# Performance work log

Measured on AMD Instinct MI355X. Metric: run time of the kernel, lower is better.

Reference implementation:

```python
import jax, jax.numpy as jnp
import numpy as np

B, C, H, W, K = 8, 256, 128, 128, 19  # batch, image channels, spatial, num keypoints


def _uniform_linear(key, out_dim, in_dim):
    # torch nn.Linear default init: U(-1/sqrt(fan_in), 1/sqrt(fan_in))
    bound = 1.0 / np.sqrt(in_dim)
    kw, kb = jax.random.split(key)
    w = jax.random.uniform(kw, (out_dim, in_dim), jnp.float32, -bound, bound)
    b = jax.random.uniform(kb, (out_dim,), jnp.float32, -bound, bound)
    return w, b


def setup_inputs() -> dict:
    key = jax.random.key(0)
    ks = jax.random.split(key, 8)
    image_features = jax.random.normal(ks[0], (B, C, H, W), jnp.float32)
    # keypoints: (x, y, vis). forward computes int((x / W).clamp(0, W-1)), so
    # coords are drawn in [0, W*W) / [0, H*H) to cover the full heatmap grid.
    kx = jax.random.uniform(ks[1], (B, K), jnp.float32, 0.0, float(W * W))
    ky = jax.random.uniform(ks[2], (B, K), jnp.float32, 0.0, float(H * H))
    vis = jax.random.uniform(ks[3], (B, K), jnp.float32)  # >0 => visible
    keypoint_features = jnp.stack([kx, ky, vis], axis=-1)  # [B,K,3]
    img_fc_w, img_fc_b = _uniform_linear(ks[4], C, C)
    kp_proj_w, kp_proj_b = _uniform_linear(ks[5], K, K)  # 1x1 conv == K->K linear over channels
    kp_fc_w, kp_fc_b = _uniform_linear(ks[6], C, K)
    attn_fc_w, attn_fc_b = _uniform_linear(ks[7], 1, C)
    return {
        "image_features": image_features,
        "keypoint_features": keypoint_features,
        "img_fc_w": img_fc_w, "img_fc_b": img_fc_b,
        "kp_proj_w": kp_proj_w, "kp_proj_b": kp_proj_b,
        "kp_fc_w": kp_fc_w, "kp_fc_b": kp_fc_b,
        "attn_fc_w": attn_fc_w, "attn_fc_b": attn_fc_b,
    }


def keypoints_to_heatmap(keypoints, Hh, Ww):
    # Vectorized version of the original nested Python double-loop scatter.
    bsz, nkp, _ = keypoints.shape
    vis = (keypoints[:, :, 2] > 0).astype(jnp.float32)            # [B,K]
    # clamp to [0, dim-1] then truncate to int (values are >=0 so floor==trunc)
    x = jnp.clip(keypoints[:, :, 0] / Ww, 0.0, Ww - 1).astype(jnp.int32)  # [B,K]
    y = jnp.clip(keypoints[:, :, 1] / Hh, 0.0, Hh - 1).astype(jnp.int32)  # [B,K]
    bi = jnp.arange(bsz)[:, None]
    ki = jnp.arange(nkp)[None, :]
    heatmap = jnp.zeros((bsz, nkp, Hh, Ww), jnp.float32)
    # one write per (b,k) -> indices unique across writes; add of 0 for invisible kp
    return heatmap.at[bi, ki, y, x].add(vis)


def reference(image_features, keypoint_features,
              img_fc_w, img_fc_b, kp_proj_w, kp_proj_b,
              kp_fc_w, kp_fc_b, attn_fc_w, attn_fc_b):
    bsz, nch, Hh, Ww = image_features.shape
    heatmap = keypoints_to_heatmap(keypoint_features, Hh, Ww)  # [B,K,H,W]
    # F.interpolate to the same (H,W) with bilinear/align_corners=False maps
    # output pixel i -> input coord i exactly => identity; no-op.
    # keypoint_proj: 1x1 conv over K channels == per-pixel K->K linear
    kp_feat = jnp.einsum('bkhw,ok->bohw', heatmap, kp_proj_w) + kp_proj_b[None, :, None, None]
    img = image_features.reshape(bsz, nch, Hh * Ww).transpose(0, 2, 1)   # [B,S,C]
    kp = kp_feat.reshape(bsz, K, Hh * Ww).transpose(0, 2, 1)             # [B,S,K]
    img_proj = jnp.einsum('bsc,oc->bso', img, img_fc_w) + img_fc_b       # [B,S,C]
    kp_proj = jnp.einsum('bsk,ok->bso', kp, kp_fc_w) + kp_fc_b           # [B,S,C]
    combined = jnp.tanh(img_proj + kp_proj)
    scores = jax.nn.sigmoid(jnp.einsum('bsc,oc->bso', combined, attn_fc_w) + attn_fc_b)  # [B,S,1]
    attended = img * scores                                              # [B,S,C]
    return attended.transpose(0, 2, 1).reshape(bsz, nch, Hh, Ww)
```

## Files before the change

### kernel.cpp

```cpp
#include <hip/hip_runtime.h>
#include <hip/hip_bf16.h>

#define CCH 256
#define HH 128
#define WW 128
#define SS (HH*WW)
#define NB 8
#define NK 19
#define STILE 64

typedef __attribute__((ext_vector_type(8))) short short8v;
typedef __attribute__((ext_vector_type(4))) float f32x4;

static __device__ __forceinline__ unsigned short f2bf(float x) {
    __hip_bfloat16 h = __float2bfloat16(x);
    return *reinterpret_cast<unsigned short*>(&h);
}
static __device__ __forceinline__ float bf2f(unsigned short u) {
    union { unsigned int i; float f; } z; z.i = ((unsigned int)u) << 16; return z.f;
}
static __device__ __forceinline__ float tanh_fast(float x) {
    float e = __expf(2.f * x);
    return 1.f - 2.f / (e + 1.f);
}

__global__ __launch_bounds__(256) void precompute_kernel(
    const float* __restrict__ kf,
    const float* __restrict__ img_fc_w,
    const float* __restrict__ img_fc_b,
    const float* __restrict__ kp_proj_w,
    const float* __restrict__ kp_proj_b,
    const float* __restrict__ kp_fc_w,
    const float* __restrict__ kp_fc_b,
    float* __restrict__ cb,
    float* __restrict__ delta,
    int* __restrict__ pix,
    unsigned short* __restrict__ Wfrag)
{
    int t = threadIdx.x;
    {
        float acc = img_fc_b[t] + kp_fc_b[t];
        for (int k2 = 0; k2 < NK; ++k2) acc += kp_fc_w[t * NK + k2] * kp_proj_b[k2];
        cb[t] = acc;
        for (int k = 0; k < NK; ++k) {
            float d = 0.f;
            for (int k2 = 0; k2 < NK; ++k2) d += kp_fc_w[t * NK + k2] * kp_proj_w[k2 * NK + k];
            delta[t * NK + k] = d;
        }
    }
    if (t < NB * NK) {
        float kx = kf[t * 3 + 0], ky = kf[t * 3 + 1], vis = kf[t * 3 + 2];
        int p = -1;
        if (vis > 0.f) {
            int xi = (int)fminf(fmaxf(kx * (1.f / (float)WW), 0.f), (float)(WW - 1));
            int yi = (int)fminf(fmaxf(ky * (1.f / (float)HH), 0.f), (float)(HH - 1));
            p = yi * WW + xi;
        }
        pix[t] = p;
    }
    for (int g = t; g < 8 * 16 * 64; g += 256) {
        int lane = g & 63;
        int ot = (g >> 6) & 15;
        int ks = g >> 10;
        int o = ot * 16 + (lane & 15);
        int c0 = ks * 32 + (lane >> 4) * 8;
#pragma unroll
        for (int j = 0; j < 8; ++j)
            Wfrag[g * 8 + j] = f2bf(img_fc_w[o * CCH + c0 + j]);
    }
}

__global__ __launch_bounds__(256) void main_kernel(
    const float* __restrict__ img,
    const unsigned short* __restrict__ Wfrag,
    const float* __restrict__ cb,
    const float* __restrict__ aw,
    const float* __restrict__ attn_b,
    float* __restrict__ out)
{
    __shared__ unsigned short Xl[64 * 256];
    __shared__ float tmp[64 * 68];
    __shared__ float partial[4][64];
    __shared__ float scl[64];

    const int t = threadIdx.x;
    const int l = t & 63;
    const int w = t >> 6;
    const int bid = blockIdx.x;
    const int b = bid >> 8;
    const int sb = (bid & 255) * STILE;
    const float* imgb = img + (size_t)b * CCH * SS;

    for (int cc = 0; cc < 4; ++cc) {
#pragma unroll
        for (int it = 0; it < 4; ++it) {
            int idx = t + it * 256;
            int c = idx >> 4;
            int sq = idx & 15;
            const float4 v = *reinterpret_cast<const float4*>(
                imgb + (size_t)(cc * 64 + c) * SS + sb + sq * 4);
            *reinterpret_cast<float4*>(&tmp[c * 68 + sq * 4]) = v;
        }
        __syncthreads();
        {
            int s = t & 63;
            int tr = t >> 6;
#pragma unroll
            for (int half = 0; half < 2; ++half) {
                int c0 = tr * 16 + half * 8;
                short8v pk;
#pragma unroll
                for (int j = 0; j < 8; ++j)
                    pk[j] = (short)f2bf(tmp[(c0 + j) * 68 + s]);
                int cglob = cc * 64 + c0;
                int cblk = cglob >> 3;
                int idx = s * 256 + ((cblk ^ (s & 7)) << 3);
                *reinterpret_cast<short8v*>(&Xl[idx]) = pk;
            }
        }
        __syncthreads();
    }

    f32x4 acc[4][4];
#pragma unroll
    for (int m = 0; m < 4; ++m)
#pragma unroll
        for (int n = 0; n < 4; ++n)
            acc[m][n] = (f32x4){0.f, 0.f, 0.f, 0.f};

    for (int ks = 0; ks < 8; ++ks) {
        short8v a[4], bf[4];
#pragma unroll
        for (int m = 0; m < 4; ++m) {
            int ot = w * 4 + m;
            a[m] = *reinterpret_cast<const short8v*>(
                &Wfrag[(((ks * 16 + ot) * 64) + l) * 8]);
        }
#pragma unroll
        for (int n = 0; n < 4; ++n) {
            int s = n * 16 + (l & 15);
            int cblk = ks * 4 + (l >> 4);
            int idx = s * 256 + ((cblk ^ (s & 7)) << 3);
            bf[n] = *reinterpret_cast<const short8v*>(&Xl[idx]);
        }
#pragma unroll
        for (int m = 0; m < 4; ++m)
#pragma unroll
            for (int n = 0; n < 4; ++n)
                acc[m][n] = __builtin_amdgcn_mfma_f32_16x16x32_bf16(a[m], bf[n], acc[m][n], 0, 0, 0);
    }

    float cbv[4][4], awv[4][4];
#pragma unroll
    for (int m = 0; m < 4; ++m)
#pragma unroll
        for (int r = 0; r < 4; ++r) {
            int o = w * 64 + m * 16 + ((l >> 4) << 2) + r;
            cbv[m][r] = cb[o];
            awv[m][r] = aw[o];
        }
    float p[4];
#pragma unroll
    for (int n = 0; n < 4; ++n) {
        float acc_p = 0.f;
#pragma unroll
        for (int m = 0; m < 4; ++m)
#pragma unroll
            for (int r = 0; r < 4; ++r)
                acc_p += awv[m][r] * tanh_fast(acc[m][n][r] + cbv[m][r]);
        acc_p += __shfl_xor(acc_p, 16);
        acc_p += __shfl_xor(acc_p, 32);
        p[n] = acc_p;
    }
    if (l < 16) {
#pragma unroll
        for (int n = 0; n < 4; ++n) partial[w][n * 16 + l] = p[n];
    }
    __syncthreads();
    if (t < 64) {
        float z = partial[0][t] + partial[1][t] + partial[2][t] + partial[3][t] + attn_b[0];
        scl[t] = 1.f / (1.f + __expf(-z));
    }
    __syncthreads();

    float sc = scl[l];
#pragma unroll
    for (int g = 0; g < 8; ++g) {
        int cg = w * 64 + g * 8;
        int cblk = cg >> 3;
        int idx = l * 256 + ((cblk ^ (l & 7)) << 3);
        short8v v = *reinterpret_cast<const short8v*>(&Xl[idx]);
#pragma unroll
        for (int j = 0; j < 8; ++j) {
            float xv = bf2f((unsigned short)v[j]);
            out[(size_t)(b * CCH + cg + j) * SS + sb + l] = xv * sc;
        }
    }
}

__global__ __launch_bounds__(256) void fixup_kernel(
    const float* __restrict__ img,
    const float* __restrict__ img_fc_w,
    const float* __restrict__ aw,
    const float* __restrict__ attn_b,
    const float* __restrict__ cb,
    const float* __restrict__ delta,
    const int* __restrict__ pix,
    float* __restrict__ out)
{
    int bk = blockIdx.x;
    int b = bk / NK;
    int p = pix[bk];
    if (p < 0) return;
    __shared__ float x[256];
    __shared__ float red[256];
    __shared__ float ssc;
    int t = threadIdx.x;
    const float* imgb = img + (size_t)b * CCH * SS;
    x[t] = imgb[(size_t)t * SS + p];
    __syncthreads();
    float dsum = 0.f;
    for (int k2 = 0; k2 < NK; ++k2)
        if (pix[b * NK + k2] == p) dsum += delta[t * NK + k2];
    float acc = cb[t] + dsum;
    for (int c = 0; c < CCH; ++c) acc += img_fc_w[t * CCH + c] * x[c];
    red[t] = aw[t] * tanh_fast(acc);
    __syncthreads();
    for (int off = 128; off > 0; off >>= 1) {
        if (t < off) red[t] += red[t + off];
        __syncthreads();
    }
    if (t == 0) ssc = 1.f / (1.f + __expf(-(red[0] + attn_b[0])));
    __syncthreads();
    out[(size_t)(b * CCH + t) * SS + p] = x[t] * ssc;
}

extern "C" void kernel_launch(void* const* d_in, const int* in_sizes, int n_in,
                              void* d_out, int out_size, void* d_ws, size_t ws_size,
                              hipStream_t stream) {
    (void)in_sizes; (void)n_in; (void)out_size; (void)ws_size;
    const float* img       = (const float*)d_in[0];
    const float* kf        = (const float*)d_in[1];
    const float* img_fc_w  = (const float*)d_in[2];
    const float* img_fc_b  = (const float*)d_in[3];
    const float* kp_proj_w = (const float*)d_in[4];
    const float* kp_proj_b = (const float*)d_in[5];
    const float* kp_fc_w   = (const float*)d_in[6];
    const float* kp_fc_b   = (const float*)d_in[7];
    const float* attn_fc_w = (const float*)d_in[8];
    const float* attn_fc_b = (const float*)d_in[9];
    float* out = (float*)d_out;

    char* ws = (char*)d_ws;
    float* cb            = (float*)(ws);
    float* delta         = (float*)(ws + 1024);
    int*   pix           = (int*)  (ws + 20480);
    unsigned short* Wfrag = (unsigned short*)(ws + 21504);

    precompute_kernel<<<1, 256, 0, stream>>>(kf, img_fc_w, img_fc_b, kp_proj_w,
                                             kp_proj_b, kp_fc_w, kp_fc_b,
                                             cb, delta, pix, Wfrag);
    main_kernel<<<NB * (SS / STILE), 256, 0, stream>>>(img, Wfrag, cb,
                                                       attn_fc_w, attn_fc_b, out);
    fixup_kernel<<<NB * NK, 256, 0, stream>>>(img, img_fc_w, attn_fc_w, attn_fc_b,
                                              cb, delta, pix, out);
}
```

Measured before the change: 94.30 us.

## Double block size, prefetch whole image tile into registers, write fp32 output directly

The main kernel now runs 512 threads (8 waves) per block, each wave covering 32 output channels instead of 64. All global loads of the 64x256 image tile are issued up front into registers, so the whole tile is in flight at once instead of being fetched per chunk. The kept fp32 values are then reused for the final scaling with coalesced float4 stores, rather than reading back the bf16 copy. This also removes the bf16 rounding from the output. The cost is higher register pressure (32 floats held across the GEMM) and a larger reduction over 8 partial sums.

Result: slower. 99.17 us (+5.2%).

```diff
diff --git a/kernel.cpp b/kernel.cpp
--- a/kernel.cpp
+++ b/kernel.cpp
@@ -15,9 +15,6 @@
 static __device__ __forceinline__ unsigned short f2bf(float x) {
     __hip_bfloat16 h = __float2bfloat16(x);
     return *reinterpret_cast<unsigned short*>(&h);
-}
-static __device__ __forceinline__ float bf2f(unsigned short u) {
-    union { unsigned int i; float f; } z; z.i = ((unsigned int)u) << 16; return z.f;
 }
 static __device__ __forceinline__ float tanh_fast(float x) {
     float e = __expf(2.f * x);
@@ -70,7 +67,7 @@
     }
 }
 
-__global__ __launch_bounds__(256) void main_kernel(
+__global__ __launch_bounds__(512, 4) void main_kernel(
     const float* __restrict__ img,
     const unsigned short* __restrict__ Wfrag,
     const float* __restrict__ cb,
@@ -80,7 +77,7 @@
 {
     __shared__ unsigned short Xl[64 * 256];
     __shared__ float tmp[64 * 68];
-    __shared__ float partial[4][64];
+    __shared__ float partial[8][64];
     __shared__ float scl[64];
 
     const int t = threadIdx.x;
@@ -91,48 +88,51 @@
     const int sb = (bid & 255) * STILE;
     const float* imgb = img + (size_t)b * CCH * SS;
 
+    float4 xv[4][2];
+#pragma unroll
+    for (int cc = 0; cc < 4; ++cc)
+#pragma unroll
+        for (int it = 0; it < 2; ++it) {
+            int idx = t + it * 512;
+            xv[cc][it] = *reinterpret_cast<const float4*>(
+                imgb + (size_t)(cc * 64 + (idx >> 4)) * SS + sb + (idx & 15) * 4);
+        }
+
+#pragma unroll
     for (int cc = 0; cc < 4; ++cc) {
 #pragma unroll
-        for (int it = 0; it < 4; ++it) {
-            int idx = t + it * 256;
-            int c = idx >> 4;
-            int sq = idx & 15;
-            const float4 v = *reinterpret_cast<const float4*>(
-                imgb + (size_t)(cc * 64 + c) * SS + sb + sq * 4);
-            *reinterpret_cast<float4*>(&tmp[c * 68 + sq * 4]) = v;
+        for (int it = 0; it < 2; ++it) {
+            int idx = t + it * 512;
+            *reinterpret_cast<float4*>(&tmp[(idx >> 4) * 68 + (idx & 15) * 4]) = xv[cc][it];
         }
         __syncthreads();
         {
-            int s = t & 63;
-            int tr = t >> 6;
-#pragma unroll
-            for (int half = 0; half < 2; ++half) {
-                int c0 = tr * 16 + half * 8;
-                short8v pk;
-#pragma unroll
-                for (int j = 0; j < 8; ++j)
-                    pk[j] = (short)f2bf(tmp[(c0 + j) * 68 + s]);
-                int cglob = cc * 64 + c0;
-                int cblk = cglob >> 3;
-                int idx = s * 256 + ((cblk ^ (s & 7)) << 3);
-                *reinterpret_cast<short8v*>(&Xl[idx]) = pk;
-            }
+            int s = l;
+            int c0 = w * 8;
+            short8v pk;
+#pragma unroll
+            for (int j = 0; j < 8; ++j)
+                pk[j] = (short)f2bf(tmp[(c0 + j) * 68 + s]);
+            int cblk = cc * 8 + w;
+            int idx2 = s * 256 + ((cblk ^ (s & 7)) << 3);
+            *reinterpret_cast<short8v*>(&Xl[idx2]) = pk;
         }
         __syncthreads();
     }
 
-    f32x4 acc[4][4];
-#pragma unroll
-    for (int m = 0; m < 4; ++m)
+    f32x4 acc[2][4];
+#pragma unroll
+    for (int m = 0; m < 2; ++m)
 #pragma unroll
         for (int n = 0; n < 4; ++n)
             acc[m][n] = (f32x4){0.f, 0.f, 0.f, 0.f};
 
+#pragma unroll
     for (int ks = 0; ks < 8; ++ks) {
-        short8v a[4], bf[4];
-#pragma unroll
-        for (int m = 0; m < 4; ++m) {
-            int ot = w * 4 + m;
+        short8v a[2], bf[4];
+#pragma unroll
+        for (int m = 0; m < 2; ++m) {
+            int ot = w * 2 + m;
             a[m] = *reinterpret_cast<const short8v*>(
                 &Wfrag[(((ks * 16 + ot) * 64) + l) * 8]);
         }
@@ -144,58 +144,56 @@
             bf[n] = *reinterpret_cast<const short8v*>(&Xl[idx]);
         }
 #pragma unroll
-        for (int m = 0; m < 4; ++m)
+        for (int m = 0; m < 2; ++m)
 #pragma unroll
             for (int n = 0; n < 4; ++n)
                 acc[m][n] = __builtin_amdgcn_mfma_f32_16x16x32_bf16(a[m], bf[n], acc[m][n], 0, 0, 0);
     }
 
-    float cbv[4][4], awv[4][4];
-#pragma unroll
-    for (int m = 0; m < 4; ++m)
-#pragma unroll
-        for (int r = 0; r < 4; ++r) {
-            int o = w * 64 + m * 16 + ((l >> 4) << 2) + r;
-            cbv[m][r] = cb[o];
-            awv[m][r] = aw[o];
-        }
-    float p[4];
+    float p4[4];
 #pragma unroll
     for (int n = 0; n < 4; ++n) {
-        float acc_p = 0.f;
-#pragma unroll
-        for (int m = 0; m < 4; ++m)
-#pragma unroll
-            for (int r = 0; r < 4; ++r)
-                acc_p += awv[m][r] * tanh_fast(acc[m][n][r] + cbv[m][r]);
-        acc_p += __shfl_xor(acc_p, 16);
-        acc_p += __shfl_xor(acc_p, 32);
-        p[n] = acc_p;
+        float accp = 0.f;
+#pragma unroll
+        for (int m = 0; m < 2; ++m)
+#pragma unroll
+            for (int r = 0; r < 4; ++r) {
+                int o = (w * 2 + m) * 16 + ((l >> 4) << 2) + r;
+                accp += aw[o] * tanh_fast(acc[m][n][r] + cb[o]);
+            }
+        accp += __shfl_xor(accp, 16);
+        accp += __shfl_xor(accp, 32);
+        p4[n] = accp;
     }
     if (l < 16) {
 #pragma unroll
-        for (int n = 0; n < 4; ++n) partial[w][n * 16 + l] = p[n];
+        for (int n = 0; n < 4; ++n) partial[w][n * 16 + l] = p4[n];
     }
     __syncthreads();
     if (t < 64) {
-        float z = partial[0][t] + partial[1][t] + partial[2][t] + partial[3][t] + attn_b[0];
+        float z = attn_b[0];
+#pragma unroll
+        for (int ww = 0; ww < 8; ++ww) z += partial[ww][t];
         scl[t] = 1.f / (1.f + __expf(-z));
     }
     __syncthreads();
 
-    float sc = scl[l];
-#pragma unroll
-    for (int g = 0; g < 8; ++g) {
-        int cg = w * 64 + g * 8;
-        int cblk = cg >> 3;
-        int idx = l * 256 + ((cblk ^ (l & 7)) << 3);
-        short8v v = *reinterpret_cast<const short8v*>(&Xl[idx]);
-#pragma unroll
-        for (int j = 0; j < 8; ++j) {
-            float xv = bf2f((unsigned short)v[j]);
-            out[(size_t)(b * CCH + cg + j) * SS + sb + l] = xv * sc;
-        }
-    }
+    float4 sc4 = *reinterpret_cast<const float4*>(&scl[(l & 15) * 4]);
+#pragma unroll
+    for (int cc = 0; cc < 4; ++cc)
+#pragma unroll
+        for (int it = 0; it < 2; ++it) {
+            int idx = t + it * 512;
+            int r = cc * 64 + (idx >> 4);
+            float4 v = xv[cc][it];
+            float4 o4;
+            o4.x = v.x * sc4.x;
+            o4.y = v.y * sc4.y;
+            o4.z = v.z * sc4.z;
+            o4.w = v.w * sc4.w;
+            *reinterpret_cast<float4*>(
+                out + (size_t)(b * CCH + r) * SS + sb + (l & 15) * 4) = o4;
+        }
 }
 
 __global__ __launch_bounds__(256) void fixup_kernel(
@@ -252,15 +250,15 @@
     float* out = (float*)d_out;
 
     char* ws = (char*)d_ws;
-    float* cb            = (float*)(ws);
-    float* delta         = (float*)(ws + 1024);
-    int*   pix           = (int*)  (ws + 20480);
+    float* cb             = (float*)(ws);
+    float* delta          = (float*)(ws + 1024);
+    int*   pix            = (int*)  (ws + 20480);
     unsigned short* Wfrag = (unsigned short*)(ws + 21504);
 
     precompute_kernel<<<1, 256, 0, stream>>>(kf, img_fc_w, img_fc_b, kp_proj_w,
                                              kp_proj_b, kp_fc_w, kp_fc_b,
                                              cb, delta, pix, Wfrag);
-    main_kernel<<<NB * (SS / STILE), 256, 0, stream>>>(img, Wfrag, cb,
+    main_kernel<<<NB * (SS / STILE), 512, 0, stream>>>(img, Wfrag, cb,
                                                        attn_fc_w, attn_fc_b, out);
     fixup_kernel<<<NB * NK, 256, 0, stream>>>(img, img_fc_w, attn_fc_w, attn_fc_b,
                                               cb, delta, pix, out);
```
